# Kernel optimization log

Hardware: AMD Instinct MI355X
Metric: run time of the kernel (lower is better)

The kernel has to match this reference:

```python
import jax, jax.numpy as jnp
import numpy as np

B, T, C_IN, C_HID, C_EMB, K, MAX_DUR = 16, 512, 512, 256, 384, 5, 8
MAX_MEL = T * MAX_DUR  # static upper bound on regulated length (4096)
LRELU_SLOPE = 0.3
PAD = (K - 1) // 2
EPS = 1e-5


def setup_inputs() -> dict:
    key = jax.random.key(0)
    ks = jax.random.split(key, 14)
    s = 0.05
    return {
        "x": jax.random.normal(ks[0], (B, T, C_IN), jnp.float32),
        "x_res": jax.random.normal(ks[1], (B, T, C_IN), jnp.float32),
        "duration_target": jax.random.randint(ks[2], (B, T), 0, MAX_DUR, dtype=jnp.int32),
        "embeddings": jax.random.normal(ks[3], (B, T, C_EMB), jnp.float32),
        "src_mask": jnp.zeros((B, T), jnp.bool_),
        "conv1_w": s * jax.random.normal(ks[4], (K, C_IN, C_HID), jnp.float32),
        "conv1_b": jnp.zeros((C_HID,), jnp.float32),
        "ln1_g": jnp.ones((C_HID,), jnp.float32),
        "ln1_b": jnp.zeros((C_HID,), jnp.float32),
        "conv2_w": s * jax.random.normal(ks[5], (K, C_HID, C_HID), jnp.float32),
        "conv2_b": jnp.zeros((C_HID,), jnp.float32),
        "ln2_g": jnp.ones((C_HID,), jnp.float32),
        "ln2_b": jnp.zeros((C_HID,), jnp.float32),
        "lin_w": s * jax.random.normal(ks[6], (C_HID, 1), jnp.float32),
        "lin_b": jnp.zeros((1,), jnp.float32),
    }


def _conv1d(x, w, b):
    # x: [B, T, Cin], w: [K, Cin, Cout] -> [B, T, Cout] (same padding)
    y = jax.lax.conv_general_dilated(
        x, w, window_strides=(1,), padding=[(PAD, PAD)],
        dimension_numbers=("NWC", "WIO", "NWC"))
    return y + b


def _layer_norm(x, g, b):
    mu = jnp.mean(x, axis=-1, keepdims=True)
    var = jnp.mean(jnp.square(x - mu), axis=-1, keepdims=True)
    return (x - mu) * jax.lax.rsqrt(var + EPS) * g + b


def _duration_predictor(x, mask, c1w, c1b, g1, b1, c2w, c2b, g2, b2, lw, lb):
    h = jax.nn.leaky_relu(_conv1d(x, c1w, c1b), LRELU_SLOPE)
    h = _layer_norm(h, g1, b1)  # dropout is identity at eval
    h = jax.nn.leaky_relu(_conv1d(h, c2w, c2b), LRELU_SLOPE)
    h = _layer_norm(h, g2, b2)
    h = (h @ lw + lb).squeeze(-1)  # [B, T]
    return jnp.where(mask, 0.0, h)


def _length_regulate(x, duration):
    # Fused prefix-sum + gather replacement for the looped expand/cat/pad.
    # token i occupies output frames [cumsum[i-1], cumsum[i])
    cum = jnp.cumsum(duration, axis=1)              # [B, T]
    total = cum[:, -1]                              # [B] mel lengths
    pos = jnp.arange(MAX_MEL, dtype=cum.dtype)      # [MAX_MEL]
    idx = jax.vmap(lambda c: jnp.searchsorted(c, pos, side="right"))(cum)  # [B, MAX_MEL]
    idx = jnp.clip(idx, 0, duration.shape[1] - 1)
    valid = (pos[None, :] < total[:, None])         # [B, MAX_MEL]
    out = jnp.take_along_axis(x, idx[..., None], axis=1)
    out = out * valid[..., None].astype(x.dtype)    # zero-padded past mel_len
    return out, total.astype(jnp.int32)


def reference(x, x_res, duration_target, embeddings, src_mask,
              conv1_w, conv1_b, ln1_g, ln1_b, conv2_w, conv2_b, ln2_g, ln2_b,
              lin_w, lin_b):
    # upsample_train path: x_res is detached before the duration predictor
    x_res = jax.lax.stop_gradient(x_res)
    log_duration_prediction = _duration_predictor(
        x_res, src_mask, conv1_w, conv1_b, ln1_g, ln1_b,
        conv2_w, conv2_b, ln2_g, ln2_b, lin_w, lin_b)
    x_up, _ = _length_regulate(x, duration_target)
    emb_up, _ = _length_regulate(embeddings, duration_target)
    return x_up, log_duration_prediction, emb_up
```

## Files before the change

### kernel.cpp

```cpp
#include <hip/hip_runtime.h>


constexpr int Bn = 16, Tn = 512, CIN1 = 512, CHID = 256, CEMB = 384, MAXMEL = 4096;
constexpr int NROWS = Bn * Tn;
#define LRELU 0.3f
#define EPSV 1e-5f

typedef __attribute__((ext_vector_type(8))) short bf16x8;
typedef __attribute__((ext_vector_type(4))) float f32x4;
typedef __attribute__((ext_vector_type(16))) float f32x16;
typedef __attribute__((ext_vector_type(4))) unsigned int u32x4;
typedef unsigned short ushort_t;

static __device__ __forceinline__ ushort_t f2bf(float f) {
  unsigned u = __builtin_bit_cast(unsigned, f);
  unsigned r = (u + 0x7fffu + ((u >> 16) & 1u)) >> 16;
  return (ushort_t)r;
}

template <int CI, bool F32IN>
static __device__ __forceinline__ void conv_body(
    int mt, int ns,
    const float* __restrict__ xin, const ushort_t* __restrict__ inbf,
    const ushort_t* __restrict__ wB, float* __restrict__ hraw) {
  constexpr int NCHUNK = CI / 128;
  constexpr int ROWS = 36, LDSTRIDE = 136;
  __shared__ ushort_t sA[ROWS * LDSTRIDE];

  const int b = mt >> 4, t0 = (mt & 15) * 32;
  const int tid = threadIdx.x;
  const int l = tid & 63, nh = tid >> 6;
  const int lm = l & 31, lq = l >> 5;
  const int cob32 = ns * 4 + nh;

  f32x16 acc;
#pragma unroll
  for (int i = 0; i < 16; ++i) acc[i] = 0.f;

  const ushort_t* pB = wB + (size_t)cob32 * 512 + l * 8;

#pragma unroll 1
  for (int chunk = 0; chunk < NCHUNK; ++chunk) {
    {
      const int cibase = chunk * 128;
#pragma unroll 1
      for (int i = 0; i < 9; ++i) {
        const int p = i * 256 + tid;
        const int r = p >> 6, c2 = (p & 63) * 2;
        const int t = t0 - 2 + r;
        unsigned hv = 0;
        if ((unsigned)t < (unsigned)Tn) {
          const size_t src = (size_t)(b * Tn + t) * CI + cibase + c2;
          if (F32IN) {
            const float2 v = *(const float2*)(xin + src);
            hv = (unsigned)f2bf(v.x) | ((unsigned)f2bf(v.y) << 16);
          } else {
            hv = *(const unsigned*)(inbf + src);
          }
        }
        const int sw = ((r >> 3) & 3) << 3;
        *(unsigned*)&sA[r * LDSTRIDE + (c2 ^ sw)] = hv;
      }
    }
    __syncthreads();

#pragma unroll 1
    for (int ksh = 0; ksh < 5; ++ksh) {
      const int r = lm + ksh;
      const int sw = ((r >> 3) & 3) << 3;
      const size_t bbase = (size_t)((ksh * (CI / 16) + chunk * 8) * 8) * 512;
#pragma unroll
      for (int kk = 0; kk < 8; ++kk) {
        const int c = (kk * 16 + lq * 8) ^ sw;
        const bf16x8 a = *(const bf16x8*)&sA[r * LDSTRIDE + c];
        const bf16x8 bv = *(const bf16x8*)(pB + bbase + (size_t)kk * 8 * 512);
        acc = __builtin_amdgcn_mfma_f32_32x32x16_bf16(a, bv, acc, 0, 0, 0);
      }
    }
    __syncthreads();
  }

  const int col = ns * 128 + nh * 32 + lm;
  float* pOut = hraw + (size_t)(b * Tn + t0) * 256 + col;
#pragma unroll
  for (int reg = 0; reg < 16; ++reg) {
    const int row = (reg & 3) + 8 * (reg >> 2) + 4 * lq;
    pOut[(size_t)row * 256] = acc[reg];
  }
}

__global__ __launch_bounds__(256, 2) void conv1_gather_kernel(
    const float* __restrict__ x_res, const ushort_t* __restrict__ w1,
    float* __restrict__ hraw,
    const float* __restrict__ x, const int* __restrict__ idx,
    float* __restrict__ x_up) {
  const int blk = blockIdx.x;
  if (blk % 3 == 0) {
    const int cid = blk / 3;
    conv_body<512, true>(cid & 255, cid >> 8, x_res, nullptr, w1, hraw);
    return;
  }
  const int gid = blk - 1 - blk / 3;
  const f32x4* x4 = (const f32x4*)x;
  f32x4* xu4 = (f32x4*)x_up;
  const int tid0 = gid * 256 + threadIdx.x;
  const int stride = 1024 * 256;
  const f32x4 z = (f32x4){0.f, 0.f, 0.f, 0.f};
  for (int u = tid0; u < Bn * MAXMEL * 128; u += stride) {
    const int bp = u >> 7, i = u & 127;
    const int t = idx[bp];
    const int b = bp >> 12;
    const f32x4 v = (t >= 0) ? x4[((b << 9) + t) * 128 + i] : z;
    __builtin_nontemporal_store(v, &xu4[u]);
  }
}

__global__ __launch_bounds__(256, 2) void conv2_gather_kernel(
    const ushort_t* __restrict__ h1, const ushort_t* __restrict__ w2,
    float* __restrict__ hraw,
    const float* __restrict__ emb, const int* __restrict__ idx,
    float* __restrict__ emb_up) {
  const int blk = blockIdx.x;
  if (blk % 3 == 0) {
    const int cid = blk / 3;
    conv_body<256, false>(cid & 255, cid >> 8, nullptr, h1, w2, hraw);
    return;
  }
  const int gid = blk - 1 - blk / 3;
  const f32x4* e4 = (const f32x4*)emb;
  f32x4* eu4 = (f32x4*)emb_up;
  const int tid0 = gid * 256 + threadIdx.x;
  const int stride = 1024 * 256;
  const f32x4 z = (f32x4){0.f, 0.f, 0.f, 0.f};
  for (int u = tid0; u < Bn * MAXMEL * 96; u += stride) {
    const int bp = u / 96, i = u - bp * 96;
    const int t = idx[bp];
    const int b = bp >> 12;
    const f32x4 v = (t >= 0) ? e4[((b << 9) + t) * 96 + i] : z;
    __builtin_nontemporal_store(v, &eu4[u]);
  }
}

template <bool FINAL>
__global__ __launch_bounds__(256) void ln_kernel(
    const float* __restrict__ hraw,
    const float* __restrict__ bias, const float* __restrict__ g,
    const float* __restrict__ be, ushort_t* __restrict__ h1,
    const float* __restrict__ lw, const float* __restrict__ lb,
    const unsigned char* __restrict__ mask, float* __restrict__ ldp) {
  const int row = blockIdx.x * 4 + (threadIdx.x >> 6);
  const int l = threadIdx.x & 63;
  const f32x4 p = ((const f32x4*)hraw)[row * 64 + l];
  const f32x4 bi = ((const f32x4*)bias)[l];
  float v0 = p.x + bi.x, v1 = p.y + bi.y, v2 = p.z + bi.z, v3 = p.w + bi.w;
  v0 = (v0 > 0.f) ? v0 : LRELU * v0;
  v1 = (v1 > 0.f) ? v1 : LRELU * v1;
  v2 = (v2 > 0.f) ? v2 : LRELU * v2;
  v3 = (v3 > 0.f) ? v3 : LRELU * v3;
  float s = v0 + v1 + v2 + v3;
  float s2 = v0 * v0 + v1 * v1 + v2 * v2 + v3 * v3;
#pragma unroll
  for (int off = 32; off >= 1; off >>= 1) {
    s += __shfl_xor(s, off);
    s2 += __shfl_xor(s2, off);
  }
  const float mu = s * (1.f / 256.f);
  const float var = s2 * (1.f / 256.f) - mu * mu;
  const float rs = rsqrtf(var + EPSV);
  const f32x4 gg = ((const f32x4*)g)[l];
  const f32x4 bb = ((const f32x4*)be)[l];
  const float h0 = (v0 - mu) * rs * gg.x + bb.x;
  const float h1v = (v1 - mu) * rs * gg.y + bb.y;
  const float h2 = (v2 - mu) * rs * gg.z + bb.z;
  const float h3 = (v3 - mu) * rs * gg.w + bb.w;
  if (!FINAL) {
    ushort4 uh;
    uh.x = f2bf(h0); uh.y = f2bf(h1v); uh.z = f2bf(h2); uh.w = f2bf(h3);
    ((ushort4*)h1)[row * 64 + l] = uh;
  } else {
    const f32x4 lv = ((const f32x4*)lw)[l];
    float d = h0 * lv.x + h1v * lv.y + h2 * lv.z + h3 * lv.w;
#pragma unroll
    for (int off = 32; off >= 1; off >>= 1) d += __shfl_xor(d, off);
    if (l == 0) {
      float val = d + lb[0];
      if (mask[row]) val = 0.f;
      ldp[row] = val;
    }
  }
}

__global__ __launch_bounds__(512) void prep_kernel(
    const float* __restrict__ w1src, const float* __restrict__ w2src,
    ushort_t* __restrict__ w1dst, ushort_t* __restrict__ w2dst,
    const int* __restrict__ dur, int* __restrict__ idx) {
  __shared__ int wsum[8];
  const int blk = blockIdx.x;
  const int tid = threadIdx.x;
  if (blk < 240) {
    const float* src;
    ushort_t* dst;
    int CI, fr, sh;
    const int wv = tid >> 6, l = tid & 63;
    if (blk < 160) { src = w1src; dst = w1dst; CI = 512; sh = 5; fr = blk * 8 + wv; }
    else           { src = w2src; dst = w2dst; CI = 256; sh = 4; fr = (blk - 160) * 8 + wv; }
    const int cob32 = fr & 7;
    const int t = fr >> 3;
    const int ksh = t >> sh;
    const int ci16 = t & ((1 << sh) - 1);
    const int ci = ci16 * 16 + (l >> 5) * 8;
    const int co = cob32 * 32 + (l & 31);
    ushort_t v[8];
#pragma unroll
    for (int j = 0; j < 8; ++j)
      v[j] = f2bf(src[((size_t)(ksh * CI + ci + j)) * 256 + co]);
    u32x4 pack;
#pragma unroll
    for (int q = 0; q < 4; ++q)
      pack[q] = (unsigned)v[q * 2] | ((unsigned)v[q * 2 + 1] << 16);
    *(u32x4*)&dst[(size_t)fr * 512 + l * 8] = pack;
    return;
  }
  const int b = blk - 240;
  const int lane = tid & 63, wv = tid >> 6;
  const int d = dur[b * Tn + tid];
  int v = d;
#pragma unroll
  for (int off = 1; off <= 32; off <<= 1) {
    const int t = __shfl_up(v, off);
    if (lane >= off) v += t;
  }
  if (lane == 63) wsum[wv] = v;
  __syncthreads();
  int woff = 0, total = 0;
#pragma unroll
  for (int i = 0; i < 8; ++i) {
    const int s = wsum[i];
    if (i < wv) woff += s;
    total += s;
  }
  const int end = v + woff;
  for (int p = end - d; p < end; ++p) idx[b * MAXMEL + p] = tid;
  for (int p = total + tid; p < MAXMEL; p += 512) idx[b * MAXMEL + p] = -1;
}

extern "C" void kernel_launch(void* const* d_in, const int* in_sizes, int n_in,
                              void* d_out, int out_size, void* d_ws, size_t ws_size,
                              hipStream_t stream) {
  const float* x     = (const float*)d_in[0];
  const float* x_res = (const float*)d_in[1];
  const int*   dur   = (const int*)d_in[2];
  const float* emb   = (const float*)d_in[3];
  const unsigned char* mask = (const unsigned char*)d_in[4];
  const float* c1w = (const float*)d_in[5];
  const float* c1b = (const float*)d_in[6];
  const float* g1  = (const float*)d_in[7];
  const float* b1  = (const float*)d_in[8];
  const float* c2w = (const float*)d_in[9];
  const float* c2b = (const float*)d_in[10];
  const float* g2  = (const float*)d_in[11];
  const float* b2  = (const float*)d_in[12];
  const float* lw  = (const float*)d_in[13];
  const float* lb  = (const float*)d_in[14];

  float* x_up   = (float*)d_out;
  float* ldp    = x_up + (size_t)Bn * MAXMEL * CIN1;
  float* emb_up = ldp + (size_t)Bn * Tn;

  int* idx = (int*)d_ws;
  ushort_t* h1 = (ushort_t*)((char*)d_ws + (size_t)Bn * MAXMEL * 4);
  ushort_t* w1 = h1 + (size_t)NROWS * 256;
  ushort_t* w2 = w1 + (size_t)5 * 512 * 256;
  float* hraw = (float*)(w2 + (size_t)5 * 256 * 256);

  prep_kernel<<<256, 512, 0, stream>>>(c1w, c2w, w1, w2, dur, idx);
  conv1_gather_kernel<<<1536, 256, 0, stream>>>(
      x_res, w1, hraw, x, idx, x_up);
  ln_kernel<false><<<NROWS / 4, 256, 0, stream>>>(
      hraw, c1b, g1, b1, h1, nullptr, nullptr, nullptr, nullptr);
  conv2_gather_kernel<<<1536, 256, 0, stream>>>(
      h1, w2, hraw, emb, idx, emb_up);
  ln_kernel<true><<<NROWS / 4, 256, 0, stream>>>(
      hraw, c2b, g2, b2, nullptr, lw, lb, mask, ldp);
}
```

Before: 347.8 us.

## Fuse LayerNorm1 into conv2 tile load and drop separate LN1 kernel

The first bias+LeakyReLU+LayerNorm pass is moved into the conv2 kernel: each conv2 block reads the raw fp32 conv1 output for its 36-row halo tile, computes row statistics in LDS, normalizes, converts to bf16, and stages the full 256-channel K in one LDS tile. This removes one kernel launch and the bf16 h1 round trip through global memory. The cost is redundant LN work on halo rows and across the two N-slices, plus a larger LDS footprint. Launch bounds are also raised to 3 waves per SIMD, which may pressure registers given the 9x4 register array.

```diff
diff --git a/kernel.cpp b/kernel.cpp
--- a/kernel.cpp
+++ b/kernel.cpp
@@ -18,12 +18,10 @@
   return (ushort_t)r;
 }
 
-template <int CI, bool F32IN>
-static __device__ __forceinline__ void conv_body(
-    int mt, int ns,
-    const float* __restrict__ xin, const ushort_t* __restrict__ inbf,
+static __device__ __forceinline__ void conv1_body(
+    int mt, int ns, const float* __restrict__ xin,
     const ushort_t* __restrict__ wB, float* __restrict__ hraw) {
-  constexpr int NCHUNK = CI / 128;
+  constexpr int CI = 512;
   constexpr int ROWS = 36, LDSTRIDE = 136;
   __shared__ ushort_t sA[ROWS * LDSTRIDE];
 
@@ -40,7 +38,7 @@
   const ushort_t* pB = wB + (size_t)cob32 * 512 + l * 8;
 
 #pragma unroll 1
-  for (int chunk = 0; chunk < NCHUNK; ++chunk) {
+  for (int chunk = 0; chunk < 4; ++chunk) {
     {
       const int cibase = chunk * 128;
 #pragma unroll 1
@@ -50,13 +48,8 @@
         const int t = t0 - 2 + r;
         unsigned hv = 0;
         if ((unsigned)t < (unsigned)Tn) {
-          const size_t src = (size_t)(b * Tn + t) * CI + cibase + c2;
-          if (F32IN) {
-            const float2 v = *(const float2*)(xin + src);
-            hv = (unsigned)f2bf(v.x) | ((unsigned)f2bf(v.y) << 16);
-          } else {
-            hv = *(const unsigned*)(inbf + src);
-          }
+          const float2 v = *(const float2*)(xin + (size_t)(b * Tn + t) * CI + cibase + c2);
+          hv = (unsigned)f2bf(v.x) | ((unsigned)f2bf(v.y) << 16);
         }
         const int sw = ((r >> 3) & 3) << 3;
         *(unsigned*)&sA[r * LDSTRIDE + (c2 ^ sw)] = hv;
@@ -89,7 +82,7 @@
   }
 }
 
-__global__ __launch_bounds__(256, 2) void conv1_gather_kernel(
+__global__ __launch_bounds__(256, 3) void conv1_gather_kernel(
     const float* __restrict__ x_res, const ushort_t* __restrict__ w1,
     float* __restrict__ hraw,
     const float* __restrict__ x, const int* __restrict__ idx,
@@ -97,7 +90,7 @@
   const int blk = blockIdx.x;
   if (blk % 3 == 0) {
     const int cid = blk / 3;
-    conv_body<512, true>(cid & 255, cid >> 8, x_res, nullptr, w1, hraw);
+    conv1_body(cid & 255, cid >> 8, x_res, w1, hraw);
     return;
   }
   const int gid = blk - 1 - blk / 3;
@@ -115,42 +108,153 @@
   }
 }
 
-__global__ __launch_bounds__(256, 2) void conv2_gather_kernel(
-    const ushort_t* __restrict__ h1, const ushort_t* __restrict__ w2,
-    float* __restrict__ hraw,
+__global__ __launch_bounds__(256, 3) void conv2_gather_kernel(
+    const float* __restrict__ hraw,
+    const ushort_t* __restrict__ w2,
+    const float* __restrict__ c1b, const float* __restrict__ g1,
+    const float* __restrict__ b1, float* __restrict__ hraw2,
     const float* __restrict__ emb, const int* __restrict__ idx,
     float* __restrict__ emb_up) {
+  constexpr int CI = 256;
+  constexpr int ROWS = 36, LDSTRIDE = 264;
+  __shared__ ushort_t sA[ROWS * LDSTRIDE];
+  __shared__ float sps[ROWS * 64], spq[ROWS * 64];
+  __shared__ float sq1[ROWS * 4], sq2[ROWS * 4];
+  __shared__ float smu[ROWS], srs[ROWS];
+
   const int blk = blockIdx.x;
-  if (blk % 3 == 0) {
-    const int cid = blk / 3;
-    conv_body<256, false>(cid & 255, cid >> 8, nullptr, h1, w2, hraw);
+  if (blk % 3 != 0) {
+    const int gid = blk - 1 - blk / 3;
+    const f32x4* e4 = (const f32x4*)emb;
+    f32x4* eu4 = (f32x4*)emb_up;
+    const int tid0 = gid * 256 + threadIdx.x;
+    const int stride = 1024 * 256;
+    const f32x4 z = (f32x4){0.f, 0.f, 0.f, 0.f};
+    for (int u = tid0; u < Bn * MAXMEL * 96; u += stride) {
+      const int bp = u / 96, i = u - bp * 96;
+      const int t = idx[bp];
+      const int b = bp >> 12;
+      const f32x4 v = (t >= 0) ? e4[((b << 9) + t) * 96 + i] : z;
+      __builtin_nontemporal_store(v, &eu4[u]);
+    }
     return;
   }
-  const int gid = blk - 1 - blk / 3;
-  const f32x4* e4 = (const f32x4*)emb;
-  f32x4* eu4 = (f32x4*)emb_up;
-  const int tid0 = gid * 256 + threadIdx.x;
-  const int stride = 1024 * 256;
-  const f32x4 z = (f32x4){0.f, 0.f, 0.f, 0.f};
-  for (int u = tid0; u < Bn * MAXMEL * 96; u += stride) {
-    const int bp = u / 96, i = u - bp * 96;
-    const int t = idx[bp];
-    const int b = bp >> 12;
-    const f32x4 v = (t >= 0) ? e4[((b << 9) + t) * 96 + i] : z;
-    __builtin_nontemporal_store(v, &eu4[u]);
-  }
-}
-
-template <bool FINAL>
-__global__ __launch_bounds__(256) void ln_kernel(
-    const float* __restrict__ hraw,
-    const float* __restrict__ bias, const float* __restrict__ g,
-    const float* __restrict__ be, ushort_t* __restrict__ h1,
+
+  const int cid = blk / 3;
+  const int mt = cid & 255, ns = cid >> 8;
+  const int b = mt >> 4, t0 = (mt & 15) * 32;
+  const int tid = threadIdx.x;
+  const int l = tid & 63, nh = tid >> 6;
+  const int lm = l & 31, lq = l >> 5;
+  const int cob32 = ns * 4 + nh;
+
+  float va[9][4];
+#pragma unroll
+  for (int i = 0; i < 9; ++i) {
+    const int p = i * 256 + tid;
+    const int r = p >> 6, seg = p & 63;
+    const int t = t0 - 2 + r;
+    float s = 0.f, s2 = 0.f;
+    if ((unsigned)t < (unsigned)Tn) {
+      const f32x4 h4 = *(const f32x4*)(hraw + (size_t)(b * Tn + t) * 256 + seg * 4);
+      const f32x4 b4 = *(const f32x4*)(c1b + seg * 4);
+#pragma unroll
+      for (int q = 0; q < 4; ++q) {
+        float v = h4[q] + b4[q];
+        v = (v > 0.f) ? v : LRELU * v;
+        va[i][q] = v;
+        s += v;
+        s2 += v * v;
+      }
+    } else {
+      va[i][0] = va[i][1] = va[i][2] = va[i][3] = 0.f;
+    }
+    sps[r * 64 + seg] = s;
+    spq[r * 64 + seg] = s2;
+  }
+  __syncthreads();
+
+  if (tid < 144) {
+    const int r = tid >> 2, q = tid & 3;
+    float s = 0.f, s2 = 0.f;
+#pragma unroll
+    for (int j = 0; j < 16; ++j) {
+      s += sps[r * 64 + q * 16 + j];
+      s2 += spq[r * 64 + q * 16 + j];
+    }
+    sq1[r * 4 + q] = s;
+    sq2[r * 4 + q] = s2;
+  }
+  __syncthreads();
+  if (tid < ROWS) {
+    const float s = sq1[tid * 4] + sq1[tid * 4 + 1] + sq1[tid * 4 + 2] + sq1[tid * 4 + 3];
+    const float s2 = sq2[tid * 4] + sq2[tid * 4 + 1] + sq2[tid * 4 + 2] + sq2[tid * 4 + 3];
+    const float mu = s * (1.f / 256.f);
+    const float var = s2 * (1.f / 256.f) - mu * mu;
+    smu[tid] = mu;
+    srs[tid] = rsqrtf(var + EPSV);
+  }
+  __syncthreads();
+
+#pragma unroll
+  for (int i = 0; i < 9; ++i) {
+    const int p = i * 256 + tid;
+    const int r = p >> 6, seg = p & 63;
+    const int t = t0 - 2 + r;
+    unsigned pk0 = 0, pk1 = 0;
+    if ((unsigned)t < (unsigned)Tn) {
+      const float mu = smu[r], rs = srs[r];
+      const f32x4 g4 = *(const f32x4*)(g1 + seg * 4);
+      const f32x4 e4 = *(const f32x4*)(b1 + seg * 4);
+      const float h0 = (va[i][0] - mu) * rs * g4[0] + e4[0];
+      const float h1 = (va[i][1] - mu) * rs * g4[1] + e4[1];
+      const float h2 = (va[i][2] - mu) * rs * g4[2] + e4[2];
+      const float h3 = (va[i][3] - mu) * rs * g4[3] + e4[3];
+      pk0 = (unsigned)f2bf(h0) | ((unsigned)f2bf(h1) << 16);
+      pk1 = (unsigned)f2bf(h2) | ((unsigned)f2bf(h3) << 16);
+    }
+    const int sw = ((r >> 3) & 3) << 3;
+    const int c = (seg * 4) ^ sw;
+    *(unsigned*)&sA[r * LDSTRIDE + c] = pk0;
+    *(unsigned*)&sA[r * LDSTRIDE + c + 2] = pk1;
+  }
+  __syncthreads();
+
+  f32x16 acc;
+#pragma unroll
+  for (int i = 0; i < 16; ++i) acc[i] = 0.f;
+  const ushort_t* pB = w2 + (size_t)cob32 * 512 + l * 8;
+#pragma unroll 1
+  for (int ksh = 0; ksh < 5; ++ksh) {
+    const int r = lm + ksh;
+    const int sw = ((r >> 3) & 3) << 3;
+    const size_t bbase = (size_t)(ksh * (CI / 16) * 8) * 512;
+#pragma unroll
+    for (int kk = 0; kk < 16; ++kk) {
+      const int c = (kk * 16 + lq * 8) ^ sw;
+      const bf16x8 a = *(const bf16x8*)&sA[r * LDSTRIDE + c];
+      const bf16x8 bv = *(const bf16x8*)(pB + bbase + (size_t)kk * 8 * 512);
+      acc = __builtin_amdgcn_mfma_f32_32x32x16_bf16(a, bv, acc, 0, 0, 0);
+    }
+  }
+
+  const int col = ns * 128 + nh * 32 + lm;
+  float* pOut = hraw2 + (size_t)(b * Tn + t0) * 256 + col;
+#pragma unroll
+  for (int reg = 0; reg < 16; ++reg) {
+    const int row = (reg & 3) + 8 * (reg >> 2) + 4 * lq;
+    pOut[(size_t)row * 256] = acc[reg];
+  }
+}
+
+__global__ __launch_bounds__(256) void ln2_kernel(
+    const float* __restrict__ hraw2, const float* __restrict__ bias,
+    const float* __restrict__ g, const float* __restrict__ be,
     const float* __restrict__ lw, const float* __restrict__ lb,
     const unsigned char* __restrict__ mask, float* __restrict__ ldp) {
   const int row = blockIdx.x * 4 + (threadIdx.x >> 6);
   const int l = threadIdx.x & 63;
-  const f32x4 p = ((const f32x4*)hraw)[row * 64 + l];
+  const f32x4 p = ((const f32x4*)hraw2)[row * 64 + l];
   const f32x4 bi = ((const f32x4*)bias)[l];
   float v0 = p.x + bi.x, v1 = p.y + bi.y, v2 = p.z + bi.z, v3 = p.w + bi.w;
   v0 = (v0 > 0.f) ? v0 : LRELU * v0;
@@ -169,24 +273,17 @@
   const float rs = rsqrtf(var + EPSV);
   const f32x4 gg = ((const f32x4*)g)[l];
   const f32x4 bb = ((const f32x4*)be)[l];
-  const float h0 = (v0 - mu) * rs * gg.x + bb.x;
-  const float h1v = (v1 - mu) * rs * gg.y + bb.y;
-  const float h2 = (v2 - mu) * rs * gg.z + bb.z;
-  const float h3 = (v3 - mu) * rs * gg.w + bb.w;
-  if (!FINAL) {
-    ushort4 uh;
-    uh.x = f2bf(h0); uh.y = f2bf(h1v); uh.z = f2bf(h2); uh.w = f2bf(h3);
-    ((ushort4*)h1)[row * 64 + l] = uh;
-  } else {
-    const f32x4 lv = ((const f32x4*)lw)[l];
-    float d = h0 * lv.x + h1v * lv.y + h2 * lv.z + h3 * lv.w;
-#pragma unroll
-    for (int off = 32; off >= 1; off >>= 1) d += __shfl_xor(d, off);
-    if (l == 0) {
-      float val = d + lb[0];
-      if (mask[row]) val = 0.f;
-      ldp[row] = val;
-    }
+  const f32x4 lv = ((const f32x4*)lw)[l];
+  float d = ((v0 - mu) * rs * gg.x + bb.x) * lv.x;
+  d += ((v1 - mu) * rs * gg.y + bb.y) * lv.y;
+  d += ((v2 - mu) * rs * gg.z + bb.z) * lv.z;
+  d += ((v3 - mu) * rs * gg.w + bb.w) * lv.w;
+#pragma unroll
+  for (int off = 32; off >= 1; off >>= 1) d += __shfl_xor(d, off);
+  if (l == 0) {
+    float val = d + lb[0];
+    if (mask[row]) val = 0.f;
+    ldp[row] = val;
   }
 }
 
@@ -268,18 +365,16 @@
   float* emb_up = ldp + (size_t)Bn * Tn;
 
   int* idx = (int*)d_ws;
-  ushort_t* h1 = (ushort_t*)((char*)d_ws + (size_t)Bn * MAXMEL * 4);
-  ushort_t* w1 = h1 + (size_t)NROWS * 256;
+  ushort_t* w1 = (ushort_t*)((char*)d_ws + (size_t)Bn * MAXMEL * 4);
   ushort_t* w2 = w1 + (size_t)5 * 512 * 256;
   float* hraw = (float*)(w2 + (size_t)5 * 256 * 256);
+  float* hraw2 = hraw + (size_t)NROWS * 256;
 
   prep_kernel<<<256, 512, 0, stream>>>(c1w, c2w, w1, w2, dur, idx);
   conv1_gather_kernel<<<1536, 256, 0, stream>>>(
       x_res, w1, hraw, x, idx, x_up);
-  ln_kernel<false><<<NROWS / 4, 256, 0, stream>>>(
-      hraw, c1b, g1, b1, h1, nullptr, nullptr, nullptr, nullptr);
   conv2_gather_kernel<<<1536, 256, 0, stream>>>(
-      h1, w2, hraw, emb, idx, emb_up);
-  ln_kernel<true><<<NROWS / 4, 256, 0, stream>>>(
-      hraw, c2b, g2, b2, nullptr, lw, lb, mask, ldp);
-}
+      hraw, w2, c1b, g1, b1, hraw2, emb, idx, emb_up);
+  ln2_kernel<<<NROWS / 4, 256, 0, stream>>>(
+      hraw2, c2b, g2, b2, lw, lb, mask, ldp);
+}
```

After: 354.9 us. 1.02x slower.
